# Kernel optimization log

Hardware: AMD Instinct MI355X
Metric: run time of the kernel (lower is better)

The kernel has to match this reference:

```python
import jax, jax.numpy as jnp
import numpy as np

N = 50000      # nodes
E = 1_600_000  # edges per relation
D = 128        # input feature dim
H = 64         # gnn_hidden_channel
R = 3          # hetero relations
NEG_SLOPE = 0.2


def setup_inputs() -> dict:
    key = jax.random.key(0)
    ks = jax.random.split(key, 9)
    x = jax.random.normal(ks[0], (N, D), jnp.float32)
    edge_index = jax.random.randint(ks[1], (R, 2, E), 0, N, dtype=jnp.int32)
    edge_weight = jax.random.uniform(ks[2], (R, E), jnp.float32)
    W0 = jax.random.normal(ks[3], (R, D, H), jnp.float32) / np.float32(np.sqrt(D))
    W1 = jax.random.normal(ks[4], (R, H, H), jnp.float32) / np.float32(np.sqrt(H))
    W2 = jax.random.normal(ks[5], (R, H, H), jnp.float32) / np.float32(np.sqrt(H))
    a_src = jax.random.normal(ks[6], (R, 3, H), jnp.float32) * 0.1
    a_dst = jax.random.normal(ks[7], (R, 3, H), jnp.float32) * 0.1
    bias = jnp.zeros((R, 3, H), jnp.float32)
    return {"x": x, "edge_weight": edge_weight, "W0": W0, "W1": W1, "W2": W2,
            "a_src": a_src, "a_dst": a_dst, "bias": bias, "edge_index": edge_index}


def gat_layer(x, src, dst, ew, W, a_s, a_d, b):
    # GATConv, heads=1: h = xW; e = LeakyReLU(a_s.h_src + a_d.h_dst); softmax over dst
    h = x @ W                                  # [N, H]
    alpha_s = h @ a_s                          # [N]
    alpha_d = h @ a_d                          # [N]
    e = jax.nn.leaky_relu(alpha_s[src] + alpha_d[dst], NEG_SLOPE)  # [Etot]
    m = jax.ops.segment_max(e, dst, num_segments=N)                # per-dst max
    e = jnp.exp(e - m[dst])
    s = jax.ops.segment_sum(e, dst, num_segments=N)
    alpha = (e / (s[dst] + 1e-16)) * ew        # edge_weight scales attention
    out = jax.ops.segment_sum(alpha[:, None] * h[src], dst, num_segments=N)
    return out + b


def reference(x, edge_weight, W0, W1, W2, a_src, a_dst, bias, edge_index):
    loop = jnp.arange(N, dtype=edge_index.dtype)   # self-loops (PyG default)
    ones_w = jnp.ones((N,), x.dtype)
    outs = []
    for r in range(R):
        src = jnp.concatenate([edge_index[r, 0], loop])
        dst = jnp.concatenate([edge_index[r, 1], loop])
        ew = jnp.concatenate([edge_weight[r], ones_w])
        Ws = (W0[r], W1[r], W2[r])
        h = x
        for i in range(3):
            h = gat_layer(h, src, dst, ew, Ws[i], a_src[r, i], a_dst[r, i], bias[r, i])
            if i != 2:
                h = jax.nn.relu(h)
        outs.append(h)
    return jnp.concatenate(outs, axis=1)  # [N, R*H] = [N, 192]
```

## Files before the change

### kernel.cpp

```cpp
#include <hip/hip_runtime.h>
#include <math.h>

#define N_NODES 50000
#define E_EDGES 1600000
#define D_IN 128
#define H_DIM 64
#define R_REL 3
#define ETOT (E_EDGES + N_NODES)
#define NEG_SLOPE 0.2f

#define BSHIFT 7
#define BSIZE 128
#define NBUCK ((N_NODES + BSIZE - 1) / BSIZE)
#define CHUNK 8192
#define NBLK ((ETOT + CHUNK - 1) / CHUNK)
#define CCAP 5120

template <int DIN>
__global__ __launch_bounds__(256) void gemm_alpha_kernel(
    const float* __restrict__ xin,
    const float* __restrict__ W,
    const float* __restrict__ a_s,
    const float* __restrict__ a_d,
    float* __restrict__ h,
    float* __restrict__ as_out,
    float* __restrict__ ad_out)
{
    constexpr int KC = 64;
    constexpr int XSTR = KC + 4;
    __shared__ __align__(16) float xls[64 * XSTR];
    __shared__ __align__(16) float wls[KC * 64];
    int t = threadIdx.x;
    int n0 = blockIdx.x * 64;
    int nrows = N_NODES - n0; if (nrows > 64) nrows = 64;
    int tn = t >> 4;
    int tc = t & 15;

    float4 acc[4] = {{0,0,0,0},{0,0,0,0},{0,0,0,0},{0,0,0,0}};

    for (int kc = 0; kc < DIN; kc += KC) {
        if (kc) __syncthreads();
        int nf4 = nrows * (KC / 4);
        for (int f = t; f < nf4; f += 256) {
            int row = f >> 4;
            int q = f & 15;
            float4 xv = *reinterpret_cast<const float4*>(
                xin + (size_t)(n0 + row) * DIN + kc + q * 4);
            *reinterpret_cast<float4*>(&xls[row * XSTR + q * 4]) = xv;
        }
        for (int f = t; f < KC * 16; f += 256) {
            int kk = f >> 4;
            int q = f & 15;
            *reinterpret_cast<float4*>(&wls[kk * 64 + q * 4]) =
                *reinterpret_cast<const float4*>(W + (size_t)(kc + kk) * 64 + q * 4);
        }
        __syncthreads();

#pragma unroll
        for (int k4 = 0; k4 < KC / 4; ++k4) {
            float4 av[4], bv[4];
#pragma unroll
            for (int i = 0; i < 4; ++i)
                av[i] = *reinterpret_cast<const float4*>(
                    &xls[(tn * 4 + i) * XSTR + k4 * 4]);
#pragma unroll
            for (int u = 0; u < 4; ++u)
                bv[u] = *reinterpret_cast<const float4*>(
                    &wls[(k4 * 4 + u) * 64 + tc * 4]);
#pragma unroll
            for (int i = 0; i < 4; ++i) {
                acc[i].x = fmaf(av[i].x, bv[0].x, acc[i].x);
                acc[i].y = fmaf(av[i].x, bv[0].y, acc[i].y);
                acc[i].z = fmaf(av[i].x, bv[0].z, acc[i].z);
                acc[i].w = fmaf(av[i].x, bv[0].w, acc[i].w);
                acc[i].x = fmaf(av[i].y, bv[1].x, acc[i].x);
                acc[i].y = fmaf(av[i].y, bv[1].y, acc[i].y);
                acc[i].z = fmaf(av[i].y, bv[1].z, acc[i].z);
                acc[i].w = fmaf(av[i].y, bv[1].w, acc[i].w);
                acc[i].x = fmaf(av[i].z, bv[2].x, acc[i].x);
                acc[i].y = fmaf(av[i].z, bv[2].y, acc[i].y);
                acc[i].z = fmaf(av[i].z, bv[2].z, acc[i].z);
                acc[i].w = fmaf(av[i].z, bv[2].w, acc[i].w);
                acc[i].x = fmaf(av[i].w, bv[3].x, acc[i].x);
                acc[i].y = fmaf(av[i].w, bv[3].y, acc[i].y);
                acc[i].z = fmaf(av[i].w, bv[3].z, acc[i].z);
                acc[i].w = fmaf(av[i].w, bv[3].w, acc[i].w);
            }
        }
    }

    float4 asj = *reinterpret_cast<const float4*>(a_s + tc * 4);
    float4 adj = *reinterpret_cast<const float4*>(a_d + tc * 4);
#pragma unroll
    for (int i = 0; i < 4; ++i) {
        int node = n0 + tn * 4 + i;
        bool ok = node < N_NODES;
        if (ok)
            *reinterpret_cast<float4*>(h + (size_t)node * 64 + tc * 4) = acc[i];
        float vs = acc[i].x * asj.x + acc[i].y * asj.y +
                   acc[i].z * asj.z + acc[i].w * asj.w;
        float vd = acc[i].x * adj.x + acc[i].y * adj.y +
                   acc[i].z * adj.z + acc[i].w * adj.w;
#pragma unroll
        for (int m = 8; m >= 1; m >>= 1) {
            vs += __shfl_xor(vs, m, 64);
            vd += __shfl_xor(vd, m, 64);
        }
        if (ok && tc == 0) {
            as_out[node] = vs;
            ad_out[node] = vd;
        }
    }
}

__global__ __launch_bounds__(256) void partA_hist(const int* __restrict__ edge_index,
                                                  int* __restrict__ bh)
{
    __shared__ int hist[NBUCK];
    int t = threadIdx.x;
    int r = blockIdx.x / NBLK;
    int blk = blockIdx.x % NBLK;
    const int* dstE = edge_index + (size_t)r * 2 * E_EDGES + E_EDGES;
    for (int b = t; b < NBUCK; b += 256) hist[b] = 0;
    __syncthreads();
    int base = blk * CHUNK;
#pragma unroll 4
    for (int u = 0; u < CHUNK / 256; ++u) {
        int i = base + u * 256 + t;
        if (i < ETOT) {
            int d = (i < E_EDGES) ? dstE[i] : (i - E_EDGES);
            atomicAdd(&hist[d >> BSHIFT], 1);
        }
    }
    __syncthreads();
    int* bh_r = bh + (size_t)r * NBLK * NBUCK;
    for (int b = t; b < NBUCK; b += 256) bh_r[(size_t)blk * NBUCK + b] = hist[b];
}

__global__ __launch_bounds__(256) void partA2_scan(int* __restrict__ bh,
                                                   int* __restrict__ btot)
{
    __shared__ int tmp[256];
    int r = blockIdx.x / NBUCK;
    int b = blockIdx.x % NBUCK;
    int t = threadIdx.x;
    int* bh_r = bh + (size_t)r * NBLK * NBUCK;
    int v = (t < NBLK) ? bh_r[(size_t)t * NBUCK + b] : 0;
    int x = v;
#pragma unroll
    for (int off = 1; off < 256; off <<= 1) {
        tmp[t] = x;
        __syncthreads();
        int a = (t >= off) ? tmp[t - off] : 0;
        __syncthreads();
        x += a;
    }
    if (t < NBLK) bh_r[(size_t)t * NBUCK + b] = x - v;
    if (t == 255) btot[r * NBUCK + b] = x;
}

__global__ __launch_bounds__(256) void partA3_scan(const int* __restrict__ btot,
                                                   int* __restrict__ bbase)
{
    __shared__ int tmp[256];
    __shared__ int carry_s;
    int r = blockIdx.x;
    int t = threadIdx.x;
    const int* row = btot + r * NBUCK;
    int* outb = bbase + r * (NBUCK + 1);
    if (t == 0) carry_s = 0;
    __syncthreads();
    for (int base = 0; base < NBUCK; base += 256) {
        int idx = base + t;
        int v = (idx < NBUCK) ? row[idx] : 0;
        int x = v;
#pragma unroll
        for (int off = 1; off < 256; off <<= 1) {
            tmp[t] = x;
            __syncthreads();
            int a = (t >= off) ? tmp[t - off] : 0;
            __syncthreads();
            x += a;
        }
        int carry = carry_s;
        if (idx < NBUCK) outb[idx] = carry + x - v;
        __syncthreads();
        if (t == 255) carry_s = carry + x;
        __syncthreads();
    }
    if (t == 0) outb[NBUCK] = carry_s;
}

__global__ __launch_bounds__(256) void partB_scatter(
    const int* __restrict__ edge_index, const float* __restrict__ edge_weight,
    const int* __restrict__ bh, const int* __restrict__ bbase,
    int2* __restrict__ sedge)
{
    __shared__ int cur[NBUCK];
    int t = threadIdx.x;
    int r = blockIdx.x / NBLK;
    int blk = blockIdx.x % NBLK;
    const int* srcE = edge_index + (size_t)r * 2 * E_EDGES;
    const int* dstE = srcE + E_EDGES;
    const float* ewr = edge_weight + (size_t)r * E_EDGES;
    const int* bh_r = bh + (size_t)r * NBLK * NBUCK;
    const int* bbase_r = bbase + r * (NBUCK + 1);
    int2* se_r = sedge + (size_t)r * ETOT;
    for (int b = t; b < NBUCK; b += 256)
        cur[b] = bbase_r[b] + bh_r[(size_t)blk * NBUCK + b];
    __syncthreads();
    int base = blk * CHUNK;
#pragma unroll 4
    for (int u = 0; u < CHUNK / 256; ++u) {
        int i = base + u * 256 + t;
        if (i < ETOT) {
            int s, d;
            float w;
            if (i < E_EDGES) {
                s = srcE[i]; d = dstE[i]; w = ewr[i];
            } else {
                s = d = i - E_EDGES; w = 1.0f;
            }
            int pos = atomicAdd(&cur[d >> BSHIFT], 1);
            int2 pay;
            pay.x = s | ((d & (BSIZE - 1)) << 16);
            pay.y = __float_as_int(w);
            se_r[pos] = pay;
        }
    }
}

__global__ __launch_bounds__(256) void partC_sort(
    const int* __restrict__ bbase, int2* __restrict__ sedge,
    int* __restrict__ rs)
{
    __shared__ int2 stage[CCAP];
    __shared__ int cnt[BSIZE];
    __shared__ int rsl[BSIZE];
    __shared__ int tmp[BSIZE];
    __shared__ int cur[BSIZE];
    int r = blockIdx.x / NBUCK;
    int b = blockIdx.x % NBUCK;
    int t = threadIdx.x;
    const int* bbase_r = bbase + r * (NBUCK + 1);
    int* rs_r = rs + r * (N_NODES + 1);
    int2* se_r = sedge + (size_t)r * ETOT;
    int lo = b * BSIZE;
    int nn = N_NODES - lo; if (nn > BSIZE) nn = BSIZE;
    int seg0 = bbase_r[b], seg1 = bbase_r[b + 1];
    int len = seg1 - seg0;
    if (t < BSIZE) { cnt[t] = 0; cur[t] = 0; }
    __syncthreads();
    for (int k = t; k < len; k += 256) {
        int2 pw = se_r[seg0 + k];
        if (k < CCAP) stage[k] = pw;
        atomicAdd(&cnt[(pw.x >> 16) & (BSIZE - 1)], 1);
    }
    __syncthreads();
    int v = 0, x = 0;
    if (t < BSIZE) { v = cnt[t]; x = v; }
#pragma unroll
    for (int off = 1; off < BSIZE; off <<= 1) {
        if (t < BSIZE) tmp[t] = x;
        __syncthreads();
        int a = (t < BSIZE && t >= off) ? tmp[t - off] : 0;
        __syncthreads();
        x += a;
    }
    if (t < BSIZE) rsl[t] = x - v;
    __syncthreads();
    if (t < nn) rs_r[lo + t] = seg0 + rsl[t];
    if (b == NBUCK - 1 && t == 0) rs_r[N_NODES] = seg1;
    for (int k = t; k < len; k += 256) {
        int2 pw = (k < CCAP) ? stage[k] : se_r[seg0 + k];
        int dlo = (pw.x >> 16) & (BSIZE - 1);
        int pos = rsl[dlo] + atomicAdd(&cur[dlo], 1);
        int2 rec;
        rec.x = pw.x & 0xFFFF;
        rec.y = pw.y;
        se_r[seg0 + pos] = rec;
    }
}

__global__ __launch_bounds__(256) void agg_kernel(
    const int* __restrict__ rs, const int2* __restrict__ sedge,
    const float* __restrict__ as_v, const float* __restrict__ ad_v,
    const float* __restrict__ h,
    const float* __restrict__ bias,
    float* __restrict__ out, int out_stride, int do_relu)
{
    int wave = (int)(((size_t)blockIdx.x * blockDim.x + threadIdx.x) >> 6);
    int lane = threadIdx.x & 63;
    if (wave >= N_NODES) return;
    int beg = rs[wave], end = rs[wave + 1];
    float ad_n = ad_v[wave];

    int sub = lane >> 4;
    int f = lane & 15;
    const float* hf = h + f * 4;

    float ssum = 0.f;
    float4 a0 = {0.f, 0.f, 0.f, 0.f};
    float4 a1 = a0, a2 = a0, a3 = a0;

    for (int cbeg = beg; cbeg < end; cbeg += 64) {
        int rem = end - cbeg;
        if (rem > 64) rem = 64;
        int srcv = 0;
        float pq = 0.f;
        if (lane < rem) {
            int2 pe = sedge[cbeg + lane];
            srcv = pe.x;
            float e = as_v[srcv] + ad_n;
            e = (e > 0.f) ? e : NEG_SLOPE * e;
            float p = __expf(e);
            ssum += p;
            pq = p * __int_as_float(pe.y);
        }
        int s0 = __shfl(srcv, sub, 64);
        float q0 = __shfl(pq, sub, 64);
        int s1 = __shfl(srcv, 4 + sub, 64);
        float q1 = __shfl(pq, 4 + sub, 64);
        int s2 = __shfl(srcv, 8 + sub, 64);
        float q2 = __shfl(pq, 8 + sub, 64);
        int s3 = __shfl(srcv, 12 + sub, 64);
        float q3 = __shfl(pq, 12 + sub, 64);
        float4 h0 = *reinterpret_cast<const float4*>(hf + (size_t)s0 * 64);
        float4 h1 = *reinterpret_cast<const float4*>(hf + (size_t)s1 * 64);
        float4 h2 = *reinterpret_cast<const float4*>(hf + (size_t)s2 * 64);
        float4 h3 = *reinterpret_cast<const float4*>(hf + (size_t)s3 * 64);
        for (int t0 = 16; t0 < rem; t0 += 16) {
            int ns0 = __shfl(srcv, t0 + sub, 64);
            float nq0 = __shfl(pq, t0 + sub, 64);
            int ns1 = __shfl(srcv, t0 + 4 + sub, 64);
            float nq1 = __shfl(pq, t0 + 4 + sub, 64);
            int ns2 = __shfl(srcv, t0 + 8 + sub, 64);
            float nq2 = __shfl(pq, t0 + 8 + sub, 64);
            int ns3 = __shfl(srcv, t0 + 12 + sub, 64);
            float nq3 = __shfl(pq, t0 + 12 + sub, 64);
            float4 nh0 = *reinterpret_cast<const float4*>(hf + (size_t)ns0 * 64);
            float4 nh1 = *reinterpret_cast<const float4*>(hf + (size_t)ns1 * 64);
            float4 nh2 = *reinterpret_cast<const float4*>(hf + (size_t)ns2 * 64);
            float4 nh3 = *reinterpret_cast<const float4*>(hf + (size_t)ns3 * 64);
            a0.x = fmaf(q0, h0.x, a0.x);
            a0.y = fmaf(q0, h0.y, a0.y);
            a0.z = fmaf(q0, h0.z, a0.z);
            a0.w = fmaf(q0, h0.w, a0.w);
            a1.x = fmaf(q1, h1.x, a1.x);
            a1.y = fmaf(q1, h1.y, a1.y);
            a1.z = fmaf(q1, h1.z, a1.z);
            a1.w = fmaf(q1, h1.w, a1.w);
            a2.x = fmaf(q2, h2.x, a2.x);
            a2.y = fmaf(q2, h2.y, a2.y);
            a2.z = fmaf(q2, h2.z, a2.z);
            a2.w = fmaf(q2, h2.w, a2.w);
            a3.x = fmaf(q3, h3.x, a3.x);
            a3.y = fmaf(q3, h3.y, a3.y);
            a3.z = fmaf(q3, h3.z, a3.z);
            a3.w = fmaf(q3, h3.w, a3.w);
            q0 = nq0; h0 = nh0;
            q1 = nq1; h1 = nh1;
            q2 = nq2; h2 = nh2;
            q3 = nq3; h3 = nh3;
        }
        a0.x = fmaf(q0, h0.x, a0.x);
        a0.y = fmaf(q0, h0.y, a0.y);
        a0.z = fmaf(q0, h0.z, a0.z);
        a0.w = fmaf(q0, h0.w, a0.w);
        a1.x = fmaf(q1, h1.x, a1.x);
        a1.y = fmaf(q1, h1.y, a1.y);
        a1.z = fmaf(q1, h1.z, a1.z);
        a1.w = fmaf(q1, h1.w, a1.w);
        a2.x = fmaf(q2, h2.x, a2.x);
        a2.y = fmaf(q2, h2.y, a2.y);
        a2.z = fmaf(q2, h2.z, a2.z);
        a2.w = fmaf(q2, h2.w, a2.w);
        a3.x = fmaf(q3, h3.x, a3.x);
        a3.y = fmaf(q3, h3.y, a3.y);
        a3.z = fmaf(q3, h3.z, a3.z);
        a3.w = fmaf(q3, h3.w, a3.w);
    }

    float4 acc;
    acc.x = (a0.x + a1.x) + (a2.x + a3.x);
    acc.y = (a0.y + a1.y) + (a2.y + a3.y);
    acc.z = (a0.z + a1.z) + (a2.z + a3.z);
    acc.w = (a0.w + a1.w) + (a2.w + a3.w);

#pragma unroll
    for (int off = 32; off > 0; off >>= 1) ssum += __shfl_xor(ssum, off, 64);
    acc.x += __shfl_xor(acc.x, 16, 64);
    acc.y += __shfl_xor(acc.y, 16, 64);
    acc.z += __shfl_xor(acc.z, 16, 64);
    acc.w += __shfl_xor(acc.w, 16, 64);
    acc.x += __shfl_xor(acc.x, 32, 64);
    acc.y += __shfl_xor(acc.y, 32, 64);
    acc.z += __shfl_xor(acc.z, 32, 64);
    acc.w += __shfl_xor(acc.w, 32, 64);

    if (sub == 0) {
        float inv = 1.f / (ssum + 1e-16f);
        const float4 bv = *reinterpret_cast<const float4*>(bias + f * 4);
        float4 o;
        o.x = fmaf(acc.x, inv, bv.x);
        o.y = fmaf(acc.y, inv, bv.y);
        o.z = fmaf(acc.z, inv, bv.z);
        o.w = fmaf(acc.w, inv, bv.w);
        if (do_relu) {
            o.x = fmaxf(o.x, 0.f);
            o.y = fmaxf(o.y, 0.f);
            o.z = fmaxf(o.z, 0.f);
            o.w = fmaxf(o.w, 0.f);
        }
        *reinterpret_cast<float4*>(out + (size_t)wave * out_stride + f * 4) = o;
    }
}

extern "C" void kernel_launch(void* const* d_in, const int* in_sizes, int n_in,
                              void* d_out, int out_size, void* d_ws, size_t ws_size,
                              hipStream_t stream)
{
    (void)in_sizes; (void)n_in; (void)out_size; (void)ws_size;
    const float* x = (const float*)d_in[0];
    const float* edge_weight = (const float*)d_in[1];
    const float* W0 = (const float*)d_in[2];
    const float* W1 = (const float*)d_in[3];
    const float* W2 = (const float*)d_in[4];
    const float* a_src = (const float*)d_in[5];
    const float* a_dst = (const float*)d_in[6];
    const float* bias = (const float*)d_in[7];
    const int* edge_index = (const int*)d_in[8];
    float* out = (float*)d_out;

    char* ws = (char*)d_ws;
    size_t off = 0;
    auto alloc = [&](size_t bytes) {
        void* p = ws + off;
        off += (bytes + 255) & ~(size_t)255;
        return p;
    };
    int2* sedge = (int2*)alloc((size_t)R_REL * ETOT * 8);
    int* bh = (int*)alloc((size_t)R_REL * NBLK * NBUCK * 4);
    int* btot = (int*)alloc((size_t)R_REL * NBUCK * 4);
    int* bbase = (int*)alloc((size_t)R_REL * (NBUCK + 1) * 4);
    int* rs = (int*)alloc((size_t)R_REL * (N_NODES + 1) * 4);
    float* hbuf = (float*)alloc((size_t)N_NODES * 64 * 4);
    float* xbuf = (float*)alloc((size_t)N_NODES * 64 * 4);
    float* asv = (float*)alloc((size_t)N_NODES * 4);
    float* adv = (float*)alloc((size_t)N_NODES * 4);

    const int WAVE_BLOCKS = (N_NODES * 64 + 255) / 256;
    const int GEMM_BLOCKS = (N_NODES + 63) / 64;

    partA_hist<<<R_REL * NBLK, 256, 0, stream>>>(edge_index, bh);
    partA2_scan<<<R_REL * NBUCK, 256, 0, stream>>>(bh, btot);
    partA3_scan<<<R_REL, 256, 0, stream>>>(btot, bbase);
    partB_scatter<<<R_REL * NBLK, 256, 0, stream>>>(edge_index, edge_weight, bh, bbase, sedge);
    partC_sort<<<R_REL * NBUCK, 256, 0, stream>>>(bbase, sedge, rs);

    for (int r = 0; r < R_REL; ++r) {
        const int* rs_r = rs + r * (N_NODES + 1);
        const int2* se_r = sedge + (size_t)r * ETOT;

        for (int i = 0; i < 3; ++i) {
            const float* Wl = (i == 0) ? (W0 + (size_t)r * D_IN * H_DIM)
                            : (i == 1) ? (W1 + (size_t)r * H_DIM * H_DIM)
                                       : (W2 + (size_t)r * H_DIM * H_DIM);
            const float* asr = a_src + ((size_t)r * 3 + i) * H_DIM;
            const float* adr = a_dst + ((size_t)r * 3 + i) * H_DIM;
            const float* br = bias + ((size_t)r * 3 + i) * H_DIM;

            if (i == 0)
                gemm_alpha_kernel<D_IN><<<GEMM_BLOCKS, 256, 0, stream>>>(
                    x, Wl, asr, adr, hbuf, asv, adv);
            else
                gemm_alpha_kernel<H_DIM><<<GEMM_BLOCKS, 256, 0, stream>>>(
                    xbuf, Wl, asr, adr, hbuf, asv, adv);

            if (i < 2)
                agg_kernel<<<WAVE_BLOCKS, 256, 0, stream>>>(
                    rs_r, se_r, asv, adv, hbuf, br, xbuf, 64, 1);
            else
                agg_kernel<<<WAVE_BLOCKS, 256, 0, stream>>>(
                    rs_r, se_r, asv, adv, hbuf, br, out + r * 64, 192, 0);
        }
    }
}
```

Before: 833.3 us.

## Batch relations via grid.y and stage partition scatter in shared memory

The per-relation GEMM and aggregation launches are merged into single launches over a 2D grid, with one relation per blockIdx.y and per-relation buffers allocated when the workspace allows. This cuts launch count from 18 to 6 and fills the GPU better. The partition scatter now does a local bucket scan per block and stages edges in shared memory, so global writes are contiguous per bucket instead of scattered. CHUNK is lowered so the stage fits in LDS, which uses more shared memory per block, and the buffers take three times the workspace.

Measured after the change: 715.9 us. -14.1%, faster.

```diff
diff --git a/kernel.cpp b/kernel.cpp
--- a/kernel.cpp
+++ b/kernel.cpp
@@ -12,20 +12,29 @@
 #define BSHIFT 7
 #define BSIZE 128
 #define NBUCK ((N_NODES + BSIZE - 1) / BSIZE)
-#define CHUNK 8192
+#define CHUNK 7168
 #define NBLK ((ETOT + CHUNK - 1) / CHUNK)
 #define CCAP 5120
 
 template <int DIN>
 __global__ __launch_bounds__(256) void gemm_alpha_kernel(
-    const float* __restrict__ xin,
-    const float* __restrict__ W,
-    const float* __restrict__ a_s,
-    const float* __restrict__ a_d,
-    float* __restrict__ h,
-    float* __restrict__ as_out,
-    float* __restrict__ ad_out)
-{
+    const float* __restrict__ xin, size_t xin_rstride,
+    const float* __restrict__ W, size_t W_rstride,
+    const float* __restrict__ a_s, const float* __restrict__ a_d, size_t a_rstride,
+    float* __restrict__ h, size_t h_rstride,
+    float* __restrict__ as_out, float* __restrict__ ad_out, size_t v_rstride,
+    int r0)
+{
+    int rr = blockIdx.y;
+    int rW = r0 + rr;
+    xin += (size_t)rr * xin_rstride;
+    W += (size_t)rW * W_rstride;
+    a_s += (size_t)rW * a_rstride;
+    a_d += (size_t)rW * a_rstride;
+    h += (size_t)rr * h_rstride;
+    as_out += (size_t)rr * v_rstride;
+    ad_out += (size_t)rr * v_rstride;
+
     constexpr int KC = 64;
     constexpr int XSTR = KC + 4;
     __shared__ __align__(16) float xls[64 * XSTR];
@@ -133,18 +142,20 @@
         }
     }
     __syncthreads();
-    int* bh_r = bh + (size_t)r * NBLK * NBUCK;
-    for (int b = t; b < NBUCK; b += 256) bh_r[(size_t)blk * NBUCK + b] = hist[b];
-}
-
-__global__ __launch_bounds__(256) void partA2_scan(int* __restrict__ bh,
+    int* bh_blk = bh + ((size_t)r * NBLK + blk) * NBUCK;
+    for (int b = t; b < NBUCK; b += 256) bh_blk[b] = hist[b];
+}
+
+__global__ __launch_bounds__(256) void partA2_scan(const int* __restrict__ bh,
+                                                   int* __restrict__ bhoff,
                                                    int* __restrict__ btot)
 {
     __shared__ int tmp[256];
     int r = blockIdx.x / NBUCK;
     int b = blockIdx.x % NBUCK;
     int t = threadIdx.x;
-    int* bh_r = bh + (size_t)r * NBLK * NBUCK;
+    const int* bh_r = bh + (size_t)r * NBLK * NBUCK;
+    int* bhoff_r = bhoff + (size_t)r * NBLK * NBUCK;
     int v = (t < NBLK) ? bh_r[(size_t)t * NBUCK + b] : 0;
     int x = v;
 #pragma unroll
@@ -155,7 +166,7 @@
         __syncthreads();
         x += a;
     }
-    if (t < NBLK) bh_r[(size_t)t * NBUCK + b] = x - v;
+    if (t < NBLK) bhoff_r[(size_t)t * NBUCK + b] = x - v;
     if (t == 255) btot[r * NBUCK + b] = x;
 }
 
@@ -193,26 +204,55 @@
 
 __global__ __launch_bounds__(256) void partB_scatter(
     const int* __restrict__ edge_index, const float* __restrict__ edge_weight,
-    const int* __restrict__ bh, const int* __restrict__ bbase,
-    int2* __restrict__ sedge)
-{
+    const int* __restrict__ bh, const int* __restrict__ bhoff,
+    const int* __restrict__ bbase, int2* __restrict__ sedge)
+{
+    __shared__ int2 stage[CHUNK];
     __shared__ int cur[NBUCK];
+    __shared__ int gbase[NBUCK];
+    __shared__ int tmp[256];
+    __shared__ int carry_s;
     int t = threadIdx.x;
     int r = blockIdx.x / NBLK;
     int blk = blockIdx.x % NBLK;
     const int* srcE = edge_index + (size_t)r * 2 * E_EDGES;
     const int* dstE = srcE + E_EDGES;
     const float* ewr = edge_weight + (size_t)r * E_EDGES;
-    const int* bh_r = bh + (size_t)r * NBLK * NBUCK;
+    const int* bh_blk = bh + ((size_t)r * NBLK + blk) * NBUCK;
+    const int* bhoff_blk = bhoff + ((size_t)r * NBLK + blk) * NBUCK;
     const int* bbase_r = bbase + r * (NBUCK + 1);
     int2* se_r = sedge + (size_t)r * ETOT;
-    for (int b = t; b < NBUCK; b += 256)
-        cur[b] = bbase_r[b] + bh_r[(size_t)blk * NBUCK + b];
-    __syncthreads();
-    int base = blk * CHUNK;
+
+    if (t == 0) carry_s = 0;
+    __syncthreads();
+    for (int base = 0; base < NBUCK; base += 256) {
+        int idx = base + t;
+        int v = (idx < NBUCK) ? bh_blk[idx] : 0;
+        int x = v;
+#pragma unroll
+        for (int off = 1; off < 256; off <<= 1) {
+            tmp[t] = x;
+            __syncthreads();
+            int a = (t >= off) ? tmp[t - off] : 0;
+            __syncthreads();
+            x += a;
+        }
+        int carry = carry_s;
+        if (idx < NBUCK) {
+            int ls = carry + x - v;
+            cur[idx] = ls;
+            gbase[idx] = bbase_r[idx] + bhoff_blk[idx] - ls;
+        }
+        __syncthreads();
+        if (t == 255) carry_s = carry + x;
+        __syncthreads();
+    }
+
+    int base0 = blk * CHUNK;
+    int chunkLen = ETOT - base0; if (chunkLen > CHUNK) chunkLen = CHUNK;
 #pragma unroll 4
     for (int u = 0; u < CHUNK / 256; ++u) {
-        int i = base + u * 256 + t;
+        int i = base0 + u * 256 + t;
         if (i < ETOT) {
             int s, d;
             float w;
@@ -223,10 +263,16 @@
             }
             int pos = atomicAdd(&cur[d >> BSHIFT], 1);
             int2 pay;
-            pay.x = s | ((d & (BSIZE - 1)) << 16);
+            pay.x = s | (d << 16);
             pay.y = __float_as_int(w);
-            se_r[pos] = pay;
-        }
+            stage[pos] = pay;
+        }
+    }
+    __syncthreads();
+    for (int j = t; j < chunkLen; j += 256) {
+        int2 rec = stage[j];
+        int d = (int)(((unsigned)rec.x) >> 16);
+        se_r[gbase[d >> BSHIFT] + j] = rec;
     }
 }
 
@@ -284,11 +330,22 @@
 
 __global__ __launch_bounds__(256) void agg_kernel(
     const int* __restrict__ rs, const int2* __restrict__ sedge,
-    const float* __restrict__ as_v, const float* __restrict__ ad_v,
-    const float* __restrict__ h,
-    const float* __restrict__ bias,
-    float* __restrict__ out, int out_stride, int do_relu)
-{
+    const float* __restrict__ as_v, const float* __restrict__ ad_v, size_t v_rstride,
+    const float* __restrict__ h, size_t h_rstride,
+    const float* __restrict__ bias, size_t b_rstride,
+    float* __restrict__ out, size_t out_roffset, int out_stride, int do_relu,
+    int r0)
+{
+    int rr = blockIdx.y;
+    int rW = r0 + rr;
+    rs += (size_t)rW * (N_NODES + 1);
+    sedge += (size_t)rW * ETOT;
+    as_v += (size_t)rr * v_rstride;
+    ad_v += (size_t)rr * v_rstride;
+    h += (size_t)rr * h_rstride;
+    bias += (size_t)rW * b_rstride;
+    out += (size_t)rr * out_roffset;
+
     int wave = (int)(((size_t)blockIdx.x * blockDim.x + threadIdx.x) >> 6);
     int lane = threadIdx.x & 63;
     if (wave >= N_NODES) return;
@@ -420,7 +477,7 @@
                               void* d_out, int out_size, void* d_ws, size_t ws_size,
                               hipStream_t stream)
 {
-    (void)in_sizes; (void)n_in; (void)out_size; (void)ws_size;
+    (void)in_sizes; (void)n_in; (void)out_size;
     const float* x = (const float*)d_in[0];
     const float* edge_weight = (const float*)d_in[1];
     const float* W0 = (const float*)d_in[2];
@@ -441,48 +498,77 @@
     };
     int2* sedge = (int2*)alloc((size_t)R_REL * ETOT * 8);
     int* bh = (int*)alloc((size_t)R_REL * NBLK * NBUCK * 4);
+    int* bhoff = (int*)alloc((size_t)R_REL * NBLK * NBUCK * 4);
     int* btot = (int*)alloc((size_t)R_REL * NBUCK * 4);
     int* bbase = (int*)alloc((size_t)R_REL * (NBUCK + 1) * 4);
     int* rs = (int*)alloc((size_t)R_REL * (N_NODES + 1) * 4);
-    float* hbuf = (float*)alloc((size_t)N_NODES * 64 * 4);
-    float* xbuf = (float*)alloc((size_t)N_NODES * 64 * 4);
-    float* asv = (float*)alloc((size_t)N_NODES * 4);
-    float* adv = (float*)alloc((size_t)N_NODES * 4);
+
+    size_t per_rel = ((size_t)N_NODES * 64 * 4 * 2 + (size_t)N_NODES * 4 * 2 + 1024);
+    int K = (ws_size >= off + 3 * per_rel + (1 << 20)) ? 3 : 1;
+    float* hbuf = (float*)alloc((size_t)K * N_NODES * 64 * 4);
+    float* xbuf = (float*)alloc((size_t)K * N_NODES * 64 * 4);
+    float* asv = (float*)alloc((size_t)K * N_NODES * 4);
+    float* adv = (float*)alloc((size_t)K * N_NODES * 4);
 
     const int WAVE_BLOCKS = (N_NODES * 64 + 255) / 256;
     const int GEMM_BLOCKS = (N_NODES + 63) / 64;
+    const size_t HS = (size_t)N_NODES * 64;
+    const size_t VS = (size_t)N_NODES;
 
     partA_hist<<<R_REL * NBLK, 256, 0, stream>>>(edge_index, bh);
-    partA2_scan<<<R_REL * NBUCK, 256, 0, stream>>>(bh, btot);
+    partA2_scan<<<R_REL * NBUCK, 256, 0, stream>>>(bh, bhoff, btot);
     partA3_scan<<<R_REL, 256, 0, stream>>>(btot, bbase);
-    partB_scatter<<<R_REL * NBLK, 256, 0, stream>>>(edge_index, edge_weight, bh, bbase, sedge);
+    partB_scatter<<<R_REL * NBLK, 256, 0, stream>>>(edge_index, edge_weight,
+                                                    bh, bhoff, bbase, sedge);
     partC_sort<<<R_REL * NBUCK, 256, 0, stream>>>(bbase, sedge, rs);
 
-    for (int r = 0; r < R_REL; ++r) {
-        const int* rs_r = rs + r * (N_NODES + 1);
-        const int2* se_r = sedge + (size_t)r * ETOT;
-
+    if (K == 3) {
         for (int i = 0; i < 3; ++i) {
-            const float* Wl = (i == 0) ? (W0 + (size_t)r * D_IN * H_DIM)
-                            : (i == 1) ? (W1 + (size_t)r * H_DIM * H_DIM)
-                                       : (W2 + (size_t)r * H_DIM * H_DIM);
-            const float* asr = a_src + ((size_t)r * 3 + i) * H_DIM;
-            const float* adr = a_dst + ((size_t)r * 3 + i) * H_DIM;
-            const float* br = bias + ((size_t)r * 3 + i) * H_DIM;
-
             if (i == 0)
-                gemm_alpha_kernel<D_IN><<<GEMM_BLOCKS, 256, 0, stream>>>(
-                    x, Wl, asr, adr, hbuf, asv, adv);
+                gemm_alpha_kernel<D_IN><<<dim3(GEMM_BLOCKS, 3), 256, 0, stream>>>(
+                    x, 0, W0, (size_t)D_IN * H_DIM,
+                    a_src + i * H_DIM, a_dst + i * H_DIM, 3 * H_DIM,
+                    hbuf, HS, asv, adv, VS, 0);
             else
-                gemm_alpha_kernel<H_DIM><<<GEMM_BLOCKS, 256, 0, stream>>>(
-                    xbuf, Wl, asr, adr, hbuf, asv, adv);
-
+                gemm_alpha_kernel<H_DIM><<<dim3(GEMM_BLOCKS, 3), 256, 0, stream>>>(
+                    xbuf, HS, (i == 1 ? W1 : W2), (size_t)H_DIM * H_DIM,
+                    a_src + i * H_DIM, a_dst + i * H_DIM, 3 * H_DIM,
+                    hbuf, HS, asv, adv, VS, 0);
             if (i < 2)
-                agg_kernel<<<WAVE_BLOCKS, 256, 0, stream>>>(
-                    rs_r, se_r, asv, adv, hbuf, br, xbuf, 64, 1);
+                agg_kernel<<<dim3(WAVE_BLOCKS, 3), 256, 0, stream>>>(
+                    rs, sedge, asv, adv, VS, hbuf, HS,
+                    bias + i * H_DIM, 3 * H_DIM,
+                    xbuf, HS, 64, 1, 0);
             else
-                agg_kernel<<<WAVE_BLOCKS, 256, 0, stream>>>(
-                    rs_r, se_r, asv, adv, hbuf, br, out + r * 64, 192, 0);
-        }
-    }
-}
+                agg_kernel<<<dim3(WAVE_BLOCKS, 3), 256, 0, stream>>>(
+                    rs, sedge, asv, adv, VS, hbuf, HS,
+                    bias + i * H_DIM, 3 * H_DIM,
+                    out, 64, 192, 0, 0);
+        }
+    } else {
+        for (int r = 0; r < R_REL; ++r) {
+            for (int i = 0; i < 3; ++i) {
+                if (i == 0)
+                    gemm_alpha_kernel<D_IN><<<dim3(GEMM_BLOCKS, 1), 256, 0, stream>>>(
+                        x, 0, W0, (size_t)D_IN * H_DIM,
+                        a_src + i * H_DIM, a_dst + i * H_DIM, 3 * H_DIM,
+                        hbuf, 0, asv, adv, 0, r);
+                else
+                    gemm_alpha_kernel<H_DIM><<<dim3(GEMM_BLOCKS, 1), 256, 0, stream>>>(
+                        xbuf, 0, (i == 1 ? W1 : W2), (size_t)H_DIM * H_DIM,
+                        a_src + i * H_DIM, a_dst + i * H_DIM, 3 * H_DIM,
+                        hbuf, 0, asv, adv, 0, r);
+                if (i < 2)
+                    agg_kernel<<<dim3(WAVE_BLOCKS, 1), 256, 0, stream>>>(
+                        rs, sedge, asv, adv, 0, hbuf, 0,
+                        bias + i * H_DIM, 3 * H_DIM,
+                        xbuf, 0, 64, 1, r);
+                else
+                    agg_kernel<<<dim3(WAVE_BLOCKS, 1), 256, 0, stream>>>(
+                        rs, sedge, asv, adv, 0, hbuf, 0,
+                        bias + i * H_DIM, 3 * H_DIM,
+                        out + r * 64, 0, 192, 0, r);
+            }
+        }
+    }
+}
```
